# Kernel tuning notes

Hardware: AMD Instinct MI355X
Metric: run time of the kernel (lower is better)

## Reference

```python
import jax, jax.numpy as jnp
import numpy as np

DEGREE = 8


def setup_inputs() -> dict:
    key = jax.random.key(0)
    k1, k2 = jax.random.split(key)
    x = jax.random.normal(k1, (8192, 1024), dtype=jnp.float32)
    # xavier_normal-ish scale for coeffs [input_dim, output_dim, degree+1]
    std = (2.0 / (1024 + 1024)) ** 0.5
    cheby_coeffs = jax.random.normal(k2, (1024, 1024, DEGREE + 1), dtype=jnp.float32) * std
    return {"x": x, "cheby_coeffs": cheby_coeffs}


def _cheby(x, degree):
    # x: [B, I] in [-1, 1]; returns T: [B, I, degree+1]
    T = [jnp.ones_like(x), x]
    for n in range(2, degree + 1):
        T.append(2.0 * x * T[-1] - T[-2])
    return jnp.stack(T, axis=-1)


def reference(x, cheby_coeffs) -> jnp.ndarray:
    input_dim = cheby_coeffs.shape[0]
    degree = cheby_coeffs.shape[-1] - 1
    x = x.reshape(-1, input_dim)
    xmin = jnp.min(x, axis=1, keepdims=True)
    xmax = jnp.max(x, axis=1, keepdims=True)
    x = 2.0 * (x - xmin) / (xmax - xmin) - 1.0
    T = _cheby(x, degree)  # [B, I, D+1]
    y = jnp.einsum('bij,ioj->bo', T, cheby_coeffs)
    return y
```

## Files before the change

kernel.cpp:

```cpp
#include <hip/hip_runtime.h>
#include <hip/hip_bf16.h>


typedef __attribute__((ext_vector_type(8))) short bf16x8s;
typedef __attribute__((ext_vector_type(4))) float f32x4;

constexpr int BROWS = 8192;
constexpr int IDIM  = 1024;
constexpr int ODIM  = 1024;
constexpr int DEG1  = 9;
constexpr int KDIM  = IDIM * DEG1;
constexpr int KHALF = KDIM / 2;

__device__ __forceinline__ ushort f2bf(float f) {
  return ((__hip_bfloat16_raw)__float2bfloat16(f)).x;
}

__device__ __forceinline__ void gload_lds16(const void* g, void* l) {
  __builtin_amdgcn_global_load_lds(
      (const __attribute__((address_space(1))) unsigned int*)g,
      (__attribute__((address_space(3))) unsigned int*)l, 16, 0, 0);
}

__global__ __launch_bounds__(256) void build_a_kernel(const float* __restrict__ x,
                                                      __hip_bfloat16* __restrict__ A2) {
  __shared__ __align__(16) ushort Arow[KDIM];
  __shared__ float red[8];
  const int b = blockIdx.x, t = threadIdx.x, lane = t & 63, wv = t >> 6;
  const float4 v = ((const float4*)(x + (size_t)b * IDIM))[t];
  float mn = fminf(fminf(v.x, v.y), fminf(v.z, v.w));
  float mx = fmaxf(fmaxf(v.x, v.y), fmaxf(v.z, v.w));
#pragma unroll
  for (int off = 32; off >= 1; off >>= 1) {
    mn = fminf(mn, __shfl_xor(mn, off));
    mx = fmaxf(mx, __shfl_xor(mx, off));
  }
  if (lane == 0) { red[wv] = mn; red[4 + wv] = mx; }
  __syncthreads();
  mn = fminf(fminf(red[0], red[1]), fminf(red[2], red[3]));
  mx = fmaxf(fmaxf(red[4], red[5]), fmaxf(red[6], red[7]));
  const float sc = 2.0f / (mx - mn);
  const float of = -mn * sc - 1.0f;

  const float xs[4] = {v.x, v.y, v.z, v.w};
  ushort h[36];
#pragma unroll
  for (int c = 0; c < 4; ++c) {
    const float xn = fmaf(sc, xs[c], of);
    float T0 = 1.0f, T1 = xn;
    h[c * 9 + 0] = f2bf(1.0f);
    h[c * 9 + 1] = f2bf(xn);
#pragma unroll
    for (int n = 2; n < DEG1; ++n) {
      const float Tn = 2.0f * xn * T1 - T0;
      h[c * 9 + n] = f2bf(Tn);
      T0 = T1; T1 = Tn;
    }
  }
  uint2* d64 = (uint2*)(Arow + t * 36);
#pragma unroll
  for (int k = 0; k < 9; ++k)
    d64[k] = (uint2){(uint)h[4 * k] | ((uint)h[4 * k + 1] << 16),
                     (uint)h[4 * k + 2] | ((uint)h[4 * k + 3] << 16)};
  __syncthreads();
  uint4* gdst = (uint4*)(A2 + (size_t)b * KDIM);
  const uint4* lsrc = (const uint4*)Arow;
  for (int idx = t; idx < KDIM / 8; idx += 256) gdst[idx] = lsrc[idx];
}

__global__ __launch_bounds__(256) void build_b_kernel(const float* __restrict__ coeffs,
                                                      __hip_bfloat16* __restrict__ B2T) {
  __shared__ __align__(16) ushort tile[64 * 288];
  const int i0 = blockIdx.x * 32;
  const int o0 = blockIdx.y * 64;
  const int t  = threadIdx.x;
  for (int idx = t; idx < 18432; idx += 256) {
    const int i_l = idx / 576;
    const int rem = idx - i_l * 576;
    const float v = coeffs[((size_t)(i0 + i_l) * ODIM + o0) * DEG1 + rem];
    const int o_l = rem / 9;
    const int j   = rem - o_l * 9;
    tile[o_l * 288 + i_l * DEG1 + j] = f2bf(v);
  }
  __syncthreads();
  for (int idx = t; idx < 2304; idx += 256) {
    const int o_l = idx / 36;
    const int w   = idx - o_l * 36;
    uint4* gdst = (uint4*)((ushort*)B2T + (size_t)(o0 + o_l) * KDIM + i0 * DEG1);
    gdst[w] = ((const uint4*)tile)[idx];
  }
}

__global__ __launch_bounds__(512, 4) void gemm_kernel(const ushort* __restrict__ A2,
                                                      const ushort* __restrict__ B2T,
                                                      float* __restrict__ out) {
  constexpr int BK = 64;
  __shared__ __align__(16) ushort Sm[32768];
  const int t    = threadIdx.x;
  const int wave = t >> 6;
  const int lane = t & 63;
  const int g    = wave >> 2;
  const int w4   = wave & 3;
  const int wr   = w4 >> 1;
  const int wc   = w4 & 1;
  const int c16  = lane & 15;
  const int quad = lane >> 4;
  const int rowBase = blockIdx.y * 128;
  const int colBase = blockIdx.x * 128;

  ushort* As = Sm + g * 8192;
  ushort* Bs = Sm + 16384 + g * 8192;

  const int tp   = t & 255;
  const int srow = tp >> 3;
  const int scol = (tp & 7) ^ (srow & 7);
  const ushort* aB = A2  + (size_t)(rowBase + srow) * KDIM + (size_t)g * KHALF + scol * 8;
  const ushort* bB = B2T + (size_t)(colBase + srow) * KDIM + (size_t)g * KHALF + scol * 8;
  ushort* lA = As + tp * 8;
  ushort* lB = Bs + tp * 8;

  f32x4 acc[4][4];
#pragma unroll
  for (int a = 0; a < 4; ++a)
#pragma unroll
    for (int b = 0; b < 4; ++b) acc[a][b] = (f32x4){0.f, 0.f, 0.f, 0.f};

  for (int ip = 0; ip < KHALF / BK; ++ip) {
    const size_t ko = (size_t)ip * BK;
    __syncthreads();
#pragma unroll
    for (int rr = 0; rr < 4; ++rr) {
      gload_lds16(aB + (size_t)rr * 32 * KDIM + ko, lA + rr * 2048);
      gload_lds16(bB + (size_t)rr * 32 * KDIM + ko, lB + rr * 2048);
    }
    __syncthreads();

#pragma unroll
    for (int kh = 0; kh < 2; ++kh) {
      const int cx = ((kh * 4 + quad) ^ (c16 & 7)) * 8;
      bf16x8s afr[4], bfr[4];
#pragma unroll
      for (int tm = 0; tm < 4; ++tm)
        afr[tm] = *(const bf16x8s*)&As[(wr * 64 + tm * 16 + c16) * BK + cx];
#pragma unroll
      for (int tn = 0; tn < 4; ++tn)
        bfr[tn] = *(const bf16x8s*)&Bs[(wc * 64 + tn * 16 + c16) * BK + cx];
#pragma unroll
      for (int tm = 0; tm < 4; ++tm)
#pragma unroll
        for (int tn = 0; tn < 4; ++tn)
          acc[tm][tn] = __builtin_amdgcn_mfma_f32_16x16x32_bf16(afr[tm], bfr[tn],
                                                                acc[tm][tn], 0, 0, 0);
    }
  }

  __syncthreads();
  float* Ct = (float*)Sm;
  if (g == 1) {
#pragma unroll
    for (int tm = 0; tm < 4; ++tm)
#pragma unroll
      for (int tn = 0; tn < 4; ++tn) {
        const int lr0 = wr * 64 + tm * 16 + quad * 4;
        const int cl  = wc * 64 + tn * 16 + c16;
#pragma unroll
        for (int r = 0; r < 4; ++r) Ct[(lr0 + r) * 128 + cl] = acc[tm][tn][r];
      }
  }
  __syncthreads();
  if (g == 0) {
#pragma unroll
    for (int tm = 0; tm < 4; ++tm)
#pragma unroll
      for (int tn = 0; tn < 4; ++tn) {
        const int lr0 = wr * 64 + tm * 16 + quad * 4;
        const int cl  = wc * 64 + tn * 16 + c16;
#pragma unroll
        for (int r = 0; r < 4; ++r)
          out[(size_t)(rowBase + lr0 + r) * ODIM + colBase + cl] =
              acc[tm][tn][r] + Ct[(lr0 + r) * 128 + cl];
      }
  }
}

extern "C" void kernel_launch(void* const* d_in, const int* in_sizes, int n_in,
                              void* d_out, int out_size, void* d_ws, size_t ws_size,
                              hipStream_t stream) {
  const float* x      = (const float*)d_in[0];
  const float* coeffs = (const float*)d_in[1];
  float* out = (float*)d_out;

  char* ws = (char*)d_ws;
  ushort* B2T = (ushort*)ws;
  ushort* A2  = (ushort*)(ws + (size_t)ODIM * KDIM * 2);

  build_a_kernel<<<BROWS, 256, 0, stream>>>(x, (__hip_bfloat16*)A2);
  build_b_kernel<<<dim3(IDIM / 32, ODIM / 64), 256, 0, stream>>>(coeffs,
                                                                 (__hip_bfloat16*)B2T);
  gemm_kernel<<<dim3(ODIM / 128, BROWS / 128), 512, 0, stream>>>(A2, B2T, out);
}
```

Baseline: 320.8 us.

## Fold constant T0 Chebyshev term into per-output bias, shrink GEMM K by 1/9

Since T0 is always 1, the degree-0 coefficients are summed over inputs into a per-output bias vector. The GEMM K dimension then drops from 9*1024 to 8*1024, which also gives power-of-two row layouts. The A builder writes 8 bf16 terms directly to global memory without staging in LDS, and the B builder reduces the j=0 terms with LDS and global atomics. This adds a zero-init kernel and float atomics, so the bias summation order becomes nondeterministic.

Result: no change. 315.0 us (-1.8%).

```diff
diff --git a/kernel.cpp b/kernel.cpp
--- a/kernel.cpp
+++ b/kernel.cpp
@@ -9,8 +9,9 @@
 constexpr int IDIM  = 1024;
 constexpr int ODIM  = 1024;
 constexpr int DEG1  = 9;
-constexpr int KDIM  = IDIM * DEG1;
-constexpr int KHALF = KDIM / 2;
+constexpr int KP    = 8;
+constexpr int KD    = IDIM * KP;
+constexpr int KH    = KD / 2;
 
 __device__ __forceinline__ ushort f2bf(float f) {
   return ((__hip_bfloat16_raw)__float2bfloat16(f)).x;
@@ -22,12 +23,16 @@
       (__attribute__((address_space(3))) unsigned int*)l, 16, 0, 0);
 }
 
+__global__ __launch_bounds__(256) void zero_bias_kernel(float* __restrict__ bias) {
+  bias[blockIdx.x * 256 + threadIdx.x] = 0.0f;
+}
+
 __global__ __launch_bounds__(256) void build_a_kernel(const float* __restrict__ x,
-                                                      __hip_bfloat16* __restrict__ A2) {
-  __shared__ __align__(16) ushort Arow[KDIM];
+                                                      ushort* __restrict__ A2) {
   __shared__ float red[8];
   const int b = blockIdx.x, t = threadIdx.x, lane = t & 63, wv = t >> 6;
-  const float4 v = ((const float4*)(x + (size_t)b * IDIM))[t];
+  const float* xr = x + (size_t)b * IDIM;
+  const float4 v = ((const float4*)xr)[t];
   float mn = fminf(fminf(v.x, v.y), fminf(v.z, v.w));
   float mx = fmaxf(fmaxf(v.x, v.y), fmaxf(v.z, v.w));
 #pragma unroll
@@ -42,57 +47,59 @@
   const float sc = 2.0f / (mx - mn);
   const float of = -mn * sc - 1.0f;
 
-  const float xs[4] = {v.x, v.y, v.z, v.w};
-  ushort h[36];
+  uint4* adst = (uint4*)(A2 + (size_t)b * KD);
 #pragma unroll
   for (int c = 0; c < 4; ++c) {
-    const float xn = fmaf(sc, xs[c], of);
-    float T0 = 1.0f, T1 = xn;
-    h[c * 9 + 0] = f2bf(1.0f);
-    h[c * 9 + 1] = f2bf(xn);
-#pragma unroll
-    for (int n = 2; n < DEG1; ++n) {
-      const float Tn = 2.0f * xn * T1 - T0;
-      h[c * 9 + n] = f2bf(Tn);
-      T0 = T1; T1 = Tn;
-    }
-  }
-  uint2* d64 = (uint2*)(Arow + t * 36);
-#pragma unroll
-  for (int k = 0; k < 9; ++k)
-    d64[k] = (uint2){(uint)h[4 * k] | ((uint)h[4 * k + 1] << 16),
-                     (uint)h[4 * k + 2] | ((uint)h[4 * k + 3] << 16)};
-  __syncthreads();
-  uint4* gdst = (uint4*)(A2 + (size_t)b * KDIM);
-  const uint4* lsrc = (const uint4*)Arow;
-  for (int idx = t; idx < KDIM / 8; idx += 256) gdst[idx] = lsrc[idx];
+    const int i = c * 256 + t;
+    const float xn = fmaf(sc, xr[i], of);
+    const float T2 = 2.f * xn * xn - 1.f;
+    const float T3 = 2.f * xn * T2 - xn;
+    const float T4 = 2.f * xn * T3 - T2;
+    const float T5 = 2.f * xn * T4 - T3;
+    const float T6 = 2.f * xn * T5 - T4;
+    const float T7 = 2.f * xn * T6 - T5;
+    const float T8 = 2.f * xn * T7 - T6;
+    uint4 w;
+    w.x = (uint)f2bf(xn) | ((uint)f2bf(T2) << 16);
+    w.y = (uint)f2bf(T3) | ((uint)f2bf(T4) << 16);
+    w.z = (uint)f2bf(T5) | ((uint)f2bf(T6) << 16);
+    w.w = (uint)f2bf(T7) | ((uint)f2bf(T8) << 16);
+    adst[i] = w;
+  }
 }
 
 __global__ __launch_bounds__(256) void build_b_kernel(const float* __restrict__ coeffs,
-                                                      __hip_bfloat16* __restrict__ B2T) {
-  __shared__ __align__(16) ushort tile[64 * 288];
+                                                      ushort* __restrict__ B2T,
+                                                      float* __restrict__ bias) {
+  __shared__ __align__(16) ushort tile[64 * 256];
+  __shared__ float lb[64];
   const int i0 = blockIdx.x * 32;
   const int o0 = blockIdx.y * 64;
   const int t  = threadIdx.x;
+  if (t < 64) lb[t] = 0.0f;
+  __syncthreads();
   for (int idx = t; idx < 18432; idx += 256) {
     const int i_l = idx / 576;
     const int rem = idx - i_l * 576;
     const float v = coeffs[((size_t)(i0 + i_l) * ODIM + o0) * DEG1 + rem];
     const int o_l = rem / 9;
     const int j   = rem - o_l * 9;
-    tile[o_l * 288 + i_l * DEG1 + j] = f2bf(v);
-  }
-  __syncthreads();
-  for (int idx = t; idx < 2304; idx += 256) {
-    const int o_l = idx / 36;
-    const int w   = idx - o_l * 36;
-    uint4* gdst = (uint4*)((ushort*)B2T + (size_t)(o0 + o_l) * KDIM + i0 * DEG1);
+    if (j == 0) atomicAdd(&lb[o_l], v);
+    else tile[o_l * 256 + i_l * KP + (j - 1)] = f2bf(v);
+  }
+  __syncthreads();
+  for (int idx = t; idx < 2048; idx += 256) {
+    const int o_l = idx >> 5;
+    const int w   = idx & 31;
+    uint4* gdst = (uint4*)(B2T + (size_t)(o0 + o_l) * KD + i0 * KP);
     gdst[w] = ((const uint4*)tile)[idx];
   }
+  if (t < 64) atomicAdd(&bias[o0 + t], lb[t]);
 }
 
 __global__ __launch_bounds__(512, 4) void gemm_kernel(const ushort* __restrict__ A2,
                                                       const ushort* __restrict__ B2T,
+                                                      const float* __restrict__ bias,
                                                       float* __restrict__ out) {
   constexpr int BK = 64;
   __shared__ __align__(16) ushort Sm[32768];
@@ -114,8 +121,8 @@
   const int tp   = t & 255;
   const int srow = tp >> 3;
   const int scol = (tp & 7) ^ (srow & 7);
-  const ushort* aB = A2  + (size_t)(rowBase + srow) * KDIM + (size_t)g * KHALF + scol * 8;
-  const ushort* bB = B2T + (size_t)(colBase + srow) * KDIM + (size_t)g * KHALF + scol * 8;
+  const ushort* aB = A2  + (size_t)(rowBase + srow) * KD + (size_t)g * KH + scol * 8;
+  const ushort* bB = B2T + (size_t)(colBase + srow) * KD + (size_t)g * KH + scol * 8;
   ushort* lA = As + tp * 8;
   ushort* lB = Bs + tp * 8;
 
@@ -125,13 +132,13 @@
 #pragma unroll
     for (int b = 0; b < 4; ++b) acc[a][b] = (f32x4){0.f, 0.f, 0.f, 0.f};
 
-  for (int ip = 0; ip < KHALF / BK; ++ip) {
+  for (int ip = 0; ip < KH / BK; ++ip) {
     const size_t ko = (size_t)ip * BK;
     __syncthreads();
 #pragma unroll
     for (int rr = 0; rr < 4; ++rr) {
-      gload_lds16(aB + (size_t)rr * 32 * KDIM + ko, lA + rr * 2048);
-      gload_lds16(bB + (size_t)rr * 32 * KDIM + ko, lB + rr * 2048);
+      gload_lds16(aB + (size_t)rr * 32 * KD + ko, lA + rr * 2048);
+      gload_lds16(bB + (size_t)rr * 32 * KD + ko, lB + rr * 2048);
     }
     __syncthreads();
 
@@ -175,10 +182,11 @@
       for (int tn = 0; tn < 4; ++tn) {
         const int lr0 = wr * 64 + tm * 16 + quad * 4;
         const int cl  = wc * 64 + tn * 16 + c16;
+        const float bv = bias[colBase + cl];
 #pragma unroll
         for (int r = 0; r < 4; ++r)
           out[(size_t)(rowBase + lr0 + r) * ODIM + colBase + cl] =
-              acc[tm][tn][r] + Ct[(lr0 + r) * 128 + cl];
+              acc[tm][tn][r] + Ct[(lr0 + r) * 128 + cl] + bv;
       }
   }
 }
@@ -191,11 +199,12 @@
   float* out = (float*)d_out;
 
   char* ws = (char*)d_ws;
-  ushort* B2T = (ushort*)ws;
-  ushort* A2  = (ushort*)(ws + (size_t)ODIM * KDIM * 2);
-
-  build_a_kernel<<<BROWS, 256, 0, stream>>>(x, (__hip_bfloat16*)A2);
-  build_b_kernel<<<dim3(IDIM / 32, ODIM / 64), 256, 0, stream>>>(coeffs,
-                                                                 (__hip_bfloat16*)B2T);
-  gemm_kernel<<<dim3(ODIM / 128, BROWS / 128), 512, 0, stream>>>(A2, B2T, out);
-}
+  float*  bias = (float*)ws;
+  ushort* B2T  = (ushort*)(ws + 65536);
+  ushort* A2   = (ushort*)(ws + 65536 + (size_t)ODIM * KD * 2);
+
+  zero_bias_kernel<<<ODIM / 256, 256, 0, stream>>>(bias);
+  build_a_kernel<<<BROWS, 256, 0, stream>>>(x, A2);
+  build_b_kernel<<<dim3(IDIM / 32, ODIM / 64), 256, 0, stream>>>(coeffs, B2T, bias);
+  gemm_kernel<<<dim3(ODIM / 128, BROWS / 128), 512, 0, stream>>>(A2, B2T, bias, out);
+}
```
